# Optimization experiments

Measured on AMD Instinct MI355X. Metric: run time of the kernel, lower is better.

## Reference

```python
import jax, jax.numpy as jnp
import numpy as np

STRIDE = 1
PAD = 1
EXTENT = 3  # kernel footprint (ceil of max tap offset), 3x3 tap grid


def setup_inputs() -> dict:
    key = jax.random.key(0)
    k1, k2 = jax.random.split(key)
    B, Cin, H, W = 8, 64, 128, 128
    Cout, K = 64, 9
    x = jax.random.normal(k1, (B, Cin, H, W), dtype=jnp.float32)
    # per-tap weights, one scalar weight per (out_ch, in_ch, tap) -- op formula is 'x * w'
    weights = jax.random.normal(k2, (Cout, Cin, K), dtype=jnp.float32) * 0.05
    # 3x3 integer grid shifted by +0.4 -> non-integer offsets => bilinear (sub-pixel) gather
    base = jnp.stack(jnp.meshgrid(jnp.arange(3.0), jnp.arange(3.0), indexing='ij'), -1).reshape(9, 2)
    tap_offsets = (base + 0.4).astype(jnp.float32)  # [K, 2] (dy, dx)
    return {"x": x, "weights": weights, "tap_offsets": tap_offsets}


def _bilinear_tap(xp, dy, dx, H_out, W_out):
    # Gather xp at (oy*stride + dy, ox*stride + dx) with separable bilinear interp.
    Hp, Wp = xp.shape[-2], xp.shape[-1]
    y = jnp.arange(H_out, dtype=xp.dtype) * STRIDE + dy
    xc = jnp.arange(W_out, dtype=xp.dtype) * STRIDE + dx
    y0 = jnp.floor(y)
    x0 = jnp.floor(xc)
    fy = (y - y0)[None, None, :, None]
    fx = (xc - x0)[None, None, None, :]
    y0i = jnp.clip(y0.astype(jnp.int32), 0, Hp - 1)
    y1i = jnp.clip(y0.astype(jnp.int32) + 1, 0, Hp - 1)
    x0i = jnp.clip(x0.astype(jnp.int32), 0, Wp - 1)
    x1i = jnp.clip(x0.astype(jnp.int32) + 1, 0, Wp - 1)
    # interp rows first: [B, C, H_out, Wp]
    ry = xp[:, :, y0i, :] * (1.0 - fy) + xp[:, :, y1i, :] * fy
    # then columns: [B, C, H_out, W_out]
    return ry[:, :, :, x0i] * (1.0 - fx) + ry[:, :, :, x1i] * fx


def reference(x, weights, tap_offsets):
    B, Cin, H, W = x.shape
    K = weights.shape[-1]
    xp = jnp.pad(x, ((0, 0), (0, 0), (PAD, PAD), (PAD, PAD)))
    H_out = (H + 2 * PAD - EXTENT) // STRIDE + 1
    W_out = (W + 2 * PAD - EXTENT) // STRIDE + 1
    # gather all taps (loop over small fixed K=9, each fully vectorized over B,C,H,W)
    taps = [_bilinear_tap(xp, tap_offsets[k, 0], tap_offsets[k, 1], H_out, W_out)
            for k in range(K)]
    g = jnp.stack(taps, 0)  # [K, B, Cin, H_out, W_out]
    # per-tap op 'x * w', accumulated over taps and input channels
    return jnp.einsum('kbiyx,oik->boyx', g, weights)  # [B, Cout, H_out, W_out]
```

## Files before the change

kernel.cpp:

```cpp
#include <hip/hip_runtime.h>


#define CIN   64
#define COUT  64
#define HH    128
#define WW    128

typedef __attribute__((ext_vector_type(8)))  short bf16x8;
typedef __attribute__((ext_vector_type(4)))  float f32x4;
typedef __attribute__((ext_vector_type(16))) float f32x16;
typedef __attribute__((ext_vector_type(4)))  unsigned int u32x4;

__device__ __forceinline__ unsigned short f2bf(float f) {
  unsigned int u = __float_as_uint(f);
  u = (u + 0x7fffu + ((u >> 16) & 1u)) >> 16;
  return (unsigned short)u;
}

__global__ void make_wb(const float* __restrict__ wgt,
                        const float* __restrict__ off,
                        unsigned short* __restrict__ wb)
{
  int id = blockIdx.x * 64 + threadIdx.x;
  int o = id >> 6, c = id & 63;
  float W16[16];
  #pragma unroll
  for (int i = 0; i < 16; ++i) W16[i] = 0.f;
  for (int k = 0; k < 9; ++k) {
    float dy = off[2*k], dx = off[2*k+1];
    float fyf = floorf(dy), fxf = floorf(dx);
    int   iy = (int)fyf,   ix = (int)fxf;
    float fy = dy - fyf,   fx = dx - fxf;
    float wk = wgt[(o*CIN + c)*9 + k];
    W16[(iy  )*4 + ix  ] += wk * (1.f-fy)*(1.f-fx);
    W16[(iy  )*4 + ix+1] += wk * (1.f-fy)*fx;
    W16[(iy+1)*4 + ix  ] += wk * fy*(1.f-fx);
    W16[(iy+1)*4 + ix+1] += wk * fy*fx;
  }
  int g = c >> 4, half = (c >> 3) & 1, j = c & 7;
  int ni = o >> 5, l31 = o & 31;
  int lane = half*32 + l31;
  for (int tap = 0; tap < 16; ++tap) {
    int h8 = tap >> 3, rs8 = tap & 7;
    wb[(size_t)((((g*2 + h8)*16) + rs8*2 + ni)*64 + lane)*8 + j] = f2bf(W16[tap]);
  }
}

constexpr int CELLS = 40;
constexpr int LPOS  = 68;

__global__ __launch_bounds__(256, 3)
void conv_mfma(const float* __restrict__ x,
               const unsigned short* __restrict__ wb,
               float* __restrict__ out)
{
  __shared__ unsigned short lt[7 * LPOS * CELLS];

  const int wg = blockIdx.x;
  const int b  = wg >> 6;
  const int y0 = ((wg >> 1) & 31) * 4;
  const int x0 = (wg & 1) * 64;
  const int t  = threadIdx.x;
  const int lane = t & 63;
  const int wave = t >> 6;
  const int l31  = lane & 31;
  const int half = lane >> 5;

  f32x16 acc[2][2];
  #pragma unroll
  for (int xh = 0; xh < 2; ++xh)
    #pragma unroll
    for (int ni = 0; ni < 2; ++ni)
      acc[xh][ni] = (f32x16)(0.f);

  const unsigned short* wl = wb + lane*8;

  #pragma unroll
  for (int p = 0; p < 2; ++p) {
    if (p) __syncthreads();

    for (int id = t; id < 28 * LPOS; id += 256) {
      int cg  = id / LPOS;
      int pos = id - cg * LPOS;
      int row = cg >> 2;
      int c8  = cg & 3;
      int gy  = y0 + row - 1;
      int gx  = x0 + pos - 1;
      bool ok = ((unsigned)gy < (unsigned)HH) && ((unsigned)gx < (unsigned)WW);
      int sgy = ok ? gy : 0, sgx = ok ? gx : 0;
      float sc = ok ? 1.f : 0.f;
      const float* ps = x + ((size_t)(b*CIN + p*32 + c8*8)*HH + sgy)*WW + sgx;
      float v[8];
      #pragma unroll
      for (int cc = 0; cc < 8; ++cc) v[cc] = ps[(size_t)cc*HH*WW] * sc;
      unsigned int pk[4];
      #pragma unroll
      for (int i = 0; i < 4; ++i)
        pk[i] = (unsigned int)f2bf(v[2*i]) | ((unsigned int)f2bf(v[2*i+1]) << 16);
      *(u32x4*)&lt[(row*LPOS + pos)*CELLS + c8*8] = *(u32x4*)pk;
    }
    __syncthreads();

    bf16x8 bcur[4], bnxt[4];
    {
      const int g = p*2;
      #pragma unroll
      for (int dt = 0; dt < 2; ++dt)
        #pragma unroll
        for (int ni = 0; ni < 2; ++ni)
          bcur[dt*2+ni] = *(const bf16x8*)(wl + (size_t)(((g*2 + 0)*16) + dt*2 + ni)*512);
    }
    #pragma unroll
    for (int ki = 0; ki < 16; ++ki) {
      if (ki < 15) {
        const int kn = ki + 1;
        const int g2n = kn >> 3, h8n = (kn >> 2) & 1, q4n = kn & 3;
        const int gn = p*2 + g2n;
        #pragma unroll
        for (int dt = 0; dt < 2; ++dt)
          #pragma unroll
          for (int ni = 0; ni < 2; ++ni)
            bnxt[dt*2+ni] = *(const bf16x8*)(wl + (size_t)(((gn*2 + h8n)*16) + (q4n*2+dt)*2 + ni)*512);
      }
      const int g2 = ki >> 3, h8 = (ki >> 2) & 1, q4 = ki & 3;
      #pragma unroll
      for (int dt = 0; dt < 2; ++dt) {
        const int tap = h8*8 + q4*2 + dt;
        const int r = tap >> 2, sx = tap & 3;
        #pragma unroll
        for (int xh = 0; xh < 2; ++xh) {
          bf16x8 afr = *(const bf16x8*)
            &lt[((wave + r)*LPOS + (xh*32 + l31 + sx))*CELLS + g2*16 + half*8];
          acc[xh][0] = __builtin_amdgcn_mfma_f32_32x32x16_bf16(afr, bcur[dt*2+0], acc[xh][0], 0, 0, 0);
          acc[xh][1] = __builtin_amdgcn_mfma_f32_32x32x16_bf16(afr, bcur[dt*2+1], acc[xh][1], 0, 0, 0);
        }
      }
      #pragma unroll
      for (int i = 0; i < 4; ++i) bcur[i] = bnxt[i];
    }
  }

  const int y = y0 + wave;
  #pragma unroll
  for (int xh = 0; xh < 2; ++xh) {
    #pragma unroll
    for (int ni = 0; ni < 2; ++ni) {
      int o = ni*32 + l31;
      float* dst = out + (((size_t)(b*COUT + o))*HH + y)*WW + x0 + xh*32 + 4*half;
      #pragma unroll
      for (int rg = 0; rg < 4; ++rg) {
        f32x4 v = (f32x4){acc[xh][ni][4*rg+0], acc[xh][ni][4*rg+1],
                          acc[xh][ni][4*rg+2], acc[xh][ni][4*rg+3]};
        *(f32x4*)(dst + 8*rg) = v;
      }
    }
  }
}

extern "C" void kernel_launch(void* const* d_in, const int* in_sizes, int n_in,
                              void* d_out, int out_size, void* d_ws, size_t ws_size,
                              hipStream_t stream)
{
  const float* x   = (const float*)d_in[0];
  const float* wgt = (const float*)d_in[1];
  const float* off = (const float*)d_in[2];
  float* out = (float*)d_out;
  unsigned short* wb = (unsigned short*)d_ws;

  make_wb<<<64, 64, 0, stream>>>(wgt, off, wb);
  conv_mfma<<<512, 256, 0, stream>>>(x, wb, out);
}
```

Before: 116.2 us.

## Double-buffer LDS staging to overlap second channel-half loads with first-half MFMA

Splits the input staging into an issue phase that loads into registers and a write phase that converts and stores to LDS. Adds a second LDS buffer so the global loads for the second 32-channel half are in flight while the first half's MFMAs run. The staging loop is fully unrolled with shift-based indexing, weight prefetch goes two steps ahead, and the block index is remapped so consecutive workgroups cover different batches. The cost is double the LDS use, 64 extra staging registers and a drop in launch bounds from 3 to 2 waves per SIMD, so occupancy falls.

Result: faster. 110.4 us (-4.9%).

```diff
diff --git a/kernel.cpp b/kernel.cpp
--- a/kernel.cpp
+++ b/kernel.cpp
@@ -48,24 +48,80 @@
 
 constexpr int CELLS = 40;
 constexpr int LPOS  = 68;
-
-__global__ __launch_bounds__(256, 3)
+constexpr int BUFS  = 7 * LPOS * CELLS;
+
+__global__ __launch_bounds__(256, 2)
 void conv_mfma(const float* __restrict__ x,
                const unsigned short* __restrict__ wb,
                float* __restrict__ out)
 {
-  __shared__ unsigned short lt[7 * LPOS * CELLS];
+  __shared__ unsigned short lt[2 * BUFS];
 
   const int wg = blockIdx.x;
-  const int b  = wg >> 6;
-  const int y0 = ((wg >> 1) & 31) * 4;
-  const int x0 = (wg & 1) * 64;
+  const int b  = wg & 7;
+  const int i6 = wg >> 3;
+  const int y0 = (i6 >> 1) * 4;
+  const int x0 = (i6 & 1) * 64;
   const int t  = threadIdx.x;
   const int lane = t & 63;
   const int wave = t >> 6;
   const int l31  = lane & 31;
   const int half = lane >> 5;
 
+  const int ecg  = t >> 2;
+  const int epos = 64 + (t & 3);
+  const bool eact = (t < 112);
+
+  auto stage_issue = [&](int p, float (&v)[8][8]) {
+    #pragma unroll
+    for (int it = 0; it < 7; ++it) {
+      int id  = it*256 + t;
+      int cg  = id >> 6;
+      int pos = id & 63;
+      int row = cg >> 2, c8 = cg & 3;
+      int gy  = y0 + row - 1;
+      int gx  = x0 + pos - 1;
+      bool ok = ((unsigned)gy < (unsigned)HH) && ((unsigned)gx < (unsigned)WW);
+      const float* ps = x + ((size_t)(b*CIN + p*32 + c8*8)*HH + (ok ? gy : 0))*WW + (ok ? gx : 0);
+      float sc = ok ? 1.f : 0.f;
+      #pragma unroll
+      for (int cc = 0; cc < 8; ++cc) v[it][cc] = ps[(size_t)cc*HH*WW] * sc;
+    }
+    {
+      int row = ecg >> 2, c8 = ecg & 3;
+      int gy  = y0 + row - 1;
+      int gx  = x0 + epos - 1;
+      bool ok = eact && ((unsigned)gy < (unsigned)HH) && ((unsigned)gx < (unsigned)WW);
+      const float* ps = x + ((size_t)(b*CIN + p*32 + c8*8)*HH + (ok ? gy : 0))*WW + (ok ? gx : 0);
+      float sc = ok ? 1.f : 0.f;
+      #pragma unroll
+      for (int cc = 0; cc < 8; ++cc) v[7][cc] = ps[(size_t)cc*HH*WW] * sc;
+    }
+  };
+
+  auto stage_write = [&](float (&v)[8][8], unsigned short* base) {
+    #pragma unroll
+    for (int it = 0; it < 7; ++it) {
+      int id  = it*256 + t;
+      int cg  = id >> 6;
+      int pos = id & 63;
+      int row = cg >> 2, c8 = cg & 3;
+      unsigned int pk[4];
+      #pragma unroll
+      for (int i = 0; i < 4; ++i)
+        pk[i] = (unsigned int)f2bf(v[it][2*i]) | ((unsigned int)f2bf(v[it][2*i+1]) << 16);
+      *(u32x4*)&base[(row*LPOS + pos)*CELLS + c8*8] = *(u32x4*)pk;
+    }
+    if (eact) {
+      int row = ecg >> 2, c8 = ecg & 3;
+      unsigned int pk[4];
+      #pragma unroll
+      for (int i = 0; i < 4; ++i)
+        pk[i] = (unsigned int)f2bf(v[7][2*i]) | ((unsigned int)f2bf(v[7][2*i+1]) << 16);
+      *(u32x4*)&base[(row*LPOS + epos)*CELLS + c8*8] = *(u32x4*)pk;
+    }
+  };
+
   f32x16 acc[2][2];
   #pragma unroll
   for (int xh = 0; xh < 2; ++xh)
@@ -75,53 +131,23 @@
 
   const unsigned short* wl = wb + lane*8;
 
-  #pragma unroll
-  for (int p = 0; p < 2; ++p) {
-    if (p) __syncthreads();
-
-    for (int id = t; id < 28 * LPOS; id += 256) {
-      int cg  = id / LPOS;
-      int pos = id - cg * LPOS;
-      int row = cg >> 2;
-      int c8  = cg & 3;
-      int gy  = y0 + row - 1;
-      int gx  = x0 + pos - 1;
-      bool ok = ((unsigned)gy < (unsigned)HH) && ((unsigned)gx < (unsigned)WW);
-      int sgy = ok ? gy : 0, sgx = ok ? gx : 0;
-      float sc = ok ? 1.f : 0.f;
-      const float* ps = x + ((size_t)(b*CIN + p*32 + c8*8)*HH + sgy)*WW + sgx;
-      float v[8];
-      #pragma unroll
-      for (int cc = 0; cc < 8; ++cc) v[cc] = ps[(size_t)cc*HH*WW] * sc;
-      unsigned int pk[4];
-      #pragma unroll
-      for (int i = 0; i < 4; ++i)
-        pk[i] = (unsigned int)f2bf(v[2*i]) | ((unsigned int)f2bf(v[2*i+1]) << 16);
-      *(u32x4*)&lt[(row*LPOS + pos)*CELLS + c8*8] = *(u32x4*)pk;
-    }
-    __syncthreads();
-
-    bf16x8 bcur[4], bnxt[4];
-    {
-      const int g = p*2;
-      #pragma unroll
-      for (int dt = 0; dt < 2; ++dt)
-        #pragma unroll
-        for (int ni = 0; ni < 2; ++ni)
-          bcur[dt*2+ni] = *(const bf16x8*)(wl + (size_t)(((g*2 + 0)*16) + dt*2 + ni)*512);
-    }
+  auto loadB = [&](int p, int ki, bf16x8 (&dst)[4]) {
+    int g2 = ki >> 3, h8 = (ki >> 2) & 1, q4 = ki & 3;
+    int g = p*2 + g2;
+    #pragma unroll
+    for (int dt = 0; dt < 2; ++dt)
+      #pragma unroll
+      for (int ni = 0; ni < 2; ++ni)
+        dst[dt*2+ni] = *(const bf16x8*)(wl + (size_t)(((g*2 + h8)*16) + (q4*2+dt)*2 + ni)*512);
+  };
+
+  auto compute = [&](int p, const unsigned short* base) {
+    bf16x8 bq[3][4];
+    loadB(p, 0, bq[0]);
+    loadB(p, 1, bq[1]);
     #pragma unroll
     for (int ki = 0; ki < 16; ++ki) {
-      if (ki < 15) {
-        const int kn = ki + 1;
-        const int g2n = kn >> 3, h8n = (kn >> 2) & 1, q4n = kn & 3;
-        const int gn = p*2 + g2n;
-        #pragma unroll
-        for (int dt = 0; dt < 2; ++dt)
-          #pragma unroll
-          for (int ni = 0; ni < 2; ++ni)
-            bnxt[dt*2+ni] = *(const bf16x8*)(wl + (size_t)(((gn*2 + h8n)*16) + (q4n*2+dt)*2 + ni)*512);
-      }
+      if (ki < 14) loadB(p, ki + 2, bq[(ki + 2) % 3]);
       const int g2 = ki >> 3, h8 = (ki >> 2) & 1, q4 = ki & 3;
       #pragma unroll
       for (int dt = 0; dt < 2; ++dt) {
@@ -130,15 +156,26 @@
         #pragma unroll
         for (int xh = 0; xh < 2; ++xh) {
           bf16x8 afr = *(const bf16x8*)
-            &lt[((wave + r)*LPOS + (xh*32 + l31 + sx))*CELLS + g2*16 + half*8];
-          acc[xh][0] = __builtin_amdgcn_mfma_f32_32x32x16_bf16(afr, bcur[dt*2+0], acc[xh][0], 0, 0, 0);
-          acc[xh][1] = __builtin_amdgcn_mfma_f32_32x32x16_bf16(afr, bcur[dt*2+1], acc[xh][1], 0, 0, 0);
+            &base[((wave + r)*LPOS + (xh*32 + l31 + sx))*CELLS + g2*16 + half*8];
+          acc[xh][0] = __builtin_amdgcn_mfma_f32_32x32x16_bf16(afr, bq[ki % 3][dt*2+0], acc[xh][0], 0, 0, 0);
+          acc[xh][1] = __builtin_amdgcn_mfma_f32_32x32x16_bf16(afr, bq[ki % 3][dt*2+1], acc[xh][1], 0, 0, 0);
         }
       }
-      #pragma unroll
-      for (int i = 0; i < 4; ++i) bcur[i] = bnxt[i];
-    }
-  }
+    }
+  };
+
+  float v0[8][8];
+  stage_issue(0, v0);
+  stage_write(v0, lt);
+  __syncthreads();
+
+  float v1[8][8];
+  stage_issue(1, v1);
+  compute(0, lt);
+  stage_write(v1, lt + BUFS);
+  __syncthreads();
+
+  compute(1, lt + BUFS);
 
   const int y = y0 + wave;
   #pragma unroll
```
